# Performance work log

Measured on AMD Instinct MI355X. Metric: run time of the kernel, lower is better.

Reference implementation:

```python
import jax, jax.numpy as jnp
import numpy as np

B, S, E, H, D = 64, 512, 512, 8, 64  # batch, n_steps, embedding_size, head_count, QKV_dim

def setup_inputs() -> dict:
    key = jax.random.key(0)
    ks = jax.random.split(key, 7)
    x = jax.random.normal(ks[0], (B, S, E), dtype=jnp.float32)
    mask = jax.random.randint(ks[1], (B, S), 0, 2).astype(jnp.float32)  # 1 = masked out
    WQ = jax.random.normal(ks[2], (H, E, D), dtype=jnp.float32) * 0.1
    WK = jax.random.normal(ks[3], (H, E, D), dtype=jnp.float32) * 0.1
    WV = jax.random.normal(ks[4], (H, E, D), dtype=jnp.float32) * 0.1
    BE = jax.random.normal(ks[5], (S, E), dtype=jnp.float32) * 0.1
    WO = jax.random.normal(ks[6], (H * D, E), dtype=jnp.float32) * 0.1
    return {"x": x, "mask": mask, "WQ": WQ, "WK": WK, "WV": WV, "BE": BE, "WO": WO}

def reference(x, mask, WQ, WK, WV, BE, WO):
    # add learned positional bias
    h = x + BE  # [B,S,E]
    # per-head projections, vectorized over heads
    Q = jnp.einsum('bse,hed->bhsd', h, WQ)
    K = jnp.einsum('bse,hed->bhsd', h, WK)
    V = jnp.einsum('bse,hed->bhsd', h, WV)
    # NOTE: original scales by sqrt(embedding_size), not sqrt(QKV_dim)
    scores = jnp.einsum('bhsd,bhtd->bhst', Q, K) / np.sqrt(E).astype(np.float32)
    # additive mask trick: mask tiled over query dim, key positions masked where mask==1
    scores = scores - mask[:, None, None, :] * 1e10
    alpha = jax.nn.softmax(scores, axis=-1)  # [B,H,S,S]
    attn = jnp.einsum('bhst,bhtd->bhsd', alpha, V)  # [B,H,S,D]
    # concat heads along feature dim -> [B,S,H*D], then output projection
    attn = jnp.transpose(attn, (0, 2, 1, 3)).reshape(x.shape[0], x.shape[1], -1)
    return attn @ WO  # [B,S,E]
```

## Files before the change

### kernel.cpp

```cpp
#include <hip/hip_runtime.h>
#include <hip/hip_bf16.h>


#define Bn 64
#define Sn 512
#define En 512
#define Hn 8
#define Dn 64

typedef __attribute__((ext_vector_type(8))) short s8v;
typedef __attribute__((ext_vector_type(4))) float f4v;

__device__ __forceinline__ unsigned short f2bf(float f) {
    union { float f; unsigned int u; } v; v.f = f;
    unsigned int u = v.u;
    u += 0x7fffu + ((u >> 16) & 1u);
    return (unsigned short)(u >> 16);
}

__device__ __forceinline__ void async16(const unsigned short* g, unsigned short* l) {
    __builtin_amdgcn_global_load_lds((const __attribute__((address_space(1))) void*)g,
                                     (__attribute__((address_space(3))) void*)l, 16, 0, 0);
}
__device__ __forceinline__ void async4(const float* g, float* l) {
    __builtin_amdgcn_global_load_lds((const __attribute__((address_space(1))) void*)g,
                                     (__attribute__((address_space(3))) void*)l, 4, 0, 0);
}

__global__ __launch_bounds__(256) void prep_h(const float* __restrict__ x,
                                              const float* __restrict__ BE,
                                              unsigned short* __restrict__ hbf) {
    int i = (blockIdx.x * 256 + threadIdx.x) * 4;
    int se = i % (Sn * En);
    float4 a = *(const float4*)(x + i);
    float4 b = *(const float4*)(BE + se);
    ushort4 o;
    o.x = f2bf(a.x + b.x); o.y = f2bf(a.y + b.y);
    o.z = f2bf(a.z + b.z); o.w = f2bf(a.w + b.w);
    *(ushort4*)(hbf + i) = o;
}

__global__ __launch_bounds__(256) void prep_w(const float* __restrict__ WQ,
                                              const float* __restrict__ WK,
                                              const float* __restrict__ WV,
                                              const float* __restrict__ WO,
                                              unsigned short* __restrict__ Wqkvt,
                                              unsigned short* __restrict__ WOt) {
    int idx = blockIdx.x * 256 + threadIdx.x;
    const int NW = 3 * Hn * Dn * En;
    if (idx < NW) {
        int e = idx & 511;
        int d = (idx >> 9) & 63;
        int h = (idx >> 15) & 7;
        int m = idx >> 18;
        const float* W = (m == 0) ? WQ : (m == 1) ? WK : WV;
        Wqkvt[idx] = f2bf(W[(h * En + e) * Dn + d]);
    } else {
        int j = idx - NW;
        int n = j & 511;
        int e = j >> 9;
        WOt[j] = f2bf(WO[n * En + e]);
    }
}

__global__ __launch_bounds__(256) void qkv_gemm(const unsigned short* __restrict__ hbf,
                                                const unsigned short* __restrict__ Wqkvt,
                                                unsigned short* __restrict__ Qo,
                                                unsigned short* __restrict__ Ko,
                                                unsigned short* __restrict__ Vt) {
    int nb = blockIdx.x, mb = blockIdx.y;
    __shared__ __align__(16) unsigned short At[128 * 64];
    __shared__ __align__(16) unsigned short Bt[128 * 64];
    int tid = threadIdx.x;
    int w = tid >> 6, lane = tid & 63, quad = lane >> 4, l16 = lane & 15;
    int wr = w >> 1, wc = w & 1;
    int lrow = lane >> 3;
    int lseg = ((lane & 7) ^ lrow) * 8;

    f4v acc[4][4];
#pragma unroll
    for (int i = 0; i < 4; i++)
#pragma unroll
        for (int n = 0; n < 4; n++) acc[i][n] = (f4v){0.f, 0.f, 0.f, 0.f};

    const unsigned short* Ag = hbf + (size_t)mb * 128 * 512;
    const unsigned short* Bg = Wqkvt + (size_t)nb * 128 * 512;

    for (int kc = 0; kc < 8; kc++) {
        __syncthreads();
#pragma unroll
        for (int i = 0; i < 4; i++) {
            int r0 = w * 32 + i * 8;
            async16(Ag + (r0 + lrow) * 512 + kc * 64 + lseg, &At[r0 * 64]);
            async16(Bg + (r0 + lrow) * 512 + kc * 64 + lseg, &Bt[r0 * 64]);
        }
        __syncthreads();
#pragma unroll
        for (int ks = 0; ks < 2; ks++) {
            int sw = ((ks * 4 + quad) ^ (l16 & 7)) * 8;
            s8v a[4], b[4];
#pragma unroll
            for (int i = 0; i < 4; i++)
                a[i] = *(const s8v*)&At[(wr * 64 + i * 16 + l16) * 64 + sw];
#pragma unroll
            for (int n = 0; n < 4; n++)
                b[n] = *(const s8v*)&Bt[(wc * 64 + n * 16 + l16) * 64 + sw];
#pragma unroll
            for (int i = 0; i < 4; i++)
#pragma unroll
                for (int n = 0; n < 4; n++)
                    acc[i][n] = __builtin_amdgcn_mfma_f32_16x16x32_bf16(a[i], b[n], acc[i][n], 0, 0, 0);
        }
    }

    int mat = nb >> 2;
    int h = (nb & 3) * 2 + wc;
    int b = mb >> 2;
    int s0 = (mb & 3) * 128 + wr * 64;
    const float qscale = 0.06375873f;

    if (mat < 2) {
        unsigned short* op = (mat == 0) ? Qo : Ko;
        float sc = (mat == 0) ? qscale : 1.0f;
#pragma unroll
        for (int i = 0; i < 4; i++)
#pragma unroll
            for (int n = 0; n < 4; n++)
#pragma unroll
                for (int r = 0; r < 4; r++) {
                    int s = s0 + i * 16 + quad * 4 + r;
                    int d = n * 16 + l16;
                    op[(size_t)((b * Hn + h) * Sn + s) * Dn + d] = f2bf(acc[i][n][r] * sc);
                }
    } else {
#pragma unroll
        for (int i = 0; i < 4; i++)
#pragma unroll
            for (int n = 0; n < 4; n++) {
                int d = n * 16 + l16;
                int s = s0 + i * 16 + quad * 4;
                ushort4 pk;
                pk.x = f2bf(acc[i][n][0]); pk.y = f2bf(acc[i][n][1]);
                pk.z = f2bf(acc[i][n][2]); pk.w = f2bf(acc[i][n][3]);
                *(ushort4*)&Vt[(size_t)((b * Hn + h) * Dn + d) * Sn + s] = pk;
            }
    }
}

__global__ __launch_bounds__(512) void attn_kernel(const unsigned short* __restrict__ Q,
                                                   const unsigned short* __restrict__ K,
                                                   const unsigned short* __restrict__ Vt,
                                                   const float* __restrict__ mask,
                                                   unsigned short* __restrict__ attn) {
    int bh = blockIdx.x;
    int h = bh & 7, b = bh >> 3;
    __shared__ __align__(16) unsigned short Kc[64 * 64];
    __shared__ __align__(16) unsigned short Vc[64 * 64];
    __shared__ __align__(16) unsigned short Ps[8][16 * 64];
    __shared__ float maskv[64];
    int tid = threadIdx.x;
    int w = tid >> 6, lane = tid & 63, quad = lane >> 4, l16 = lane & 15;
    int l7 = l16 & 7, lh = l16 >> 3;
    int q4 = (quad & 1) * 4;

    const unsigned short* Qg = Q + (size_t)(bh * Sn) * Dn;
    const unsigned short* Kg = K + (size_t)(bh * Sn) * Dn;
    const unsigned short* Vg = Vt + (size_t)(bh * Dn) * Sn;

    s8v aq[4][2];
#pragma unroll
    for (int i = 0; i < 4; i++)
#pragma unroll
        for (int ks = 0; ks < 2; ks++)
            aq[i][ks] = *(const s8v*)&Qg[((w * 4 + i) * 16 + l16) * 64 + ks * 32 + quad * 8];

    f4v acc[4][4];
    float psum[4][4];
#pragma unroll
    for (int i = 0; i < 4; i++)
#pragma unroll
        for (int n = 0; n < 4; n++) {
            acc[i][n] = (f4v){0.f, 0.f, 0.f, 0.f};
            psum[i][n] = 0.f;
        }

    int srow = w * 8 + (lane >> 3);
    int sseg = ((lane & 7) ^ (srow & 7)) * 8;
    unsigned short* kdst = &Kc[w * 512];
    unsigned short* vdst = &Vc[w * 512];

    for (int kc = 0; kc < 8; kc++) {
        __syncthreads();
        async16(Kg + (kc * 64 + srow) * 64 + sseg, kdst);
        async16(Vg + srow * 512 + kc * 64 + sseg, vdst);
        if (w == 0) async4(mask + b * Sn + kc * 64 + lane, maskv);
        __syncthreads();

        unsigned short* Pw = Ps[w];
#pragma unroll
        for (int i = 0; i < 4; i++) {
            f4v sacc[4];
#pragma unroll
            for (int n = 0; n < 4; n++) sacc[n] = (f4v){0.f, 0.f, 0.f, 0.f};
#pragma unroll
            for (int ks = 0; ks < 2; ks++) {
                int sw = ((ks * 4 + quad) ^ l7) * 8;
#pragma unroll
                for (int n = 0; n < 4; n++) {
                    s8v bk = *(const s8v*)&Kc[(n * 16 + l16) * 64 + sw];
                    sacc[n] = __builtin_amdgcn_mfma_f32_16x16x32_bf16(aq[i][ks], bk, sacc[n], 0, 0, 0);
                }
            }
#pragma unroll
            for (int n = 0; n < 4; n++) {
                float msub = maskv[n * 16 + l16] * -1.4426950409e10f;
                int colpart = n * 2 + lh;
#pragma unroll
                for (int r = 0; r < 4; r++) {
                    float p = exp2f(sacc[n][r] + msub);
                    unsigned int u = __float_as_uint(p);
                    psum[i][r] += __uint_as_float(u & 0xffff0000u);
                    Pw[(quad * 4 + r) * 64 + ((colpart ^ (q4 + r)) * 8) + l7] =
                        (unsigned short)(u >> 16);
                }
            }
#pragma unroll
            for (int ks = 0; ks < 2; ks++) {
                int sw = ((ks * 4 + quad) ^ l7) * 8;
                s8v ap = *(const s8v*)&Pw[l16 * 64 + sw];
#pragma unroll
                for (int n = 0; n < 4; n++) {
                    s8v bv = *(const s8v*)&Vc[(n * 16 + l16) * 64 + sw];
                    acc[i][n] = __builtin_amdgcn_mfma_f32_16x16x32_bf16(ap, bv, acc[i][n], 0, 0, 0);
                }
            }
        }
    }

#pragma unroll
    for (int i = 0; i < 4; i++) {
        float inv[4];
#pragma unroll
        for (int r = 0; r < 4; r++) {
            float s = psum[i][r];
#pragma unroll
            for (int off = 1; off < 16; off <<= 1) s += __shfl_xor(s, off, 64);
            inv[r] = 1.0f / s;
        }
#pragma unroll
        for (int n = 0; n < 4; n++)
#pragma unroll
            for (int r = 0; r < 4; r++) {
                int query = (w * 4 + i) * 16 + quad * 4 + r;
                int col = h * 64 + n * 16 + l16;
                attn[(size_t)(b * Sn + query) * (Hn * Dn) + col] = f2bf(acc[i][n][r] * inv[r]);
            }
    }
}

__global__ __launch_bounds__(256) void outproj(const unsigned short* __restrict__ attn,
                                               const unsigned short* __restrict__ WOt,
                                               float* __restrict__ out) {
    int nb = blockIdx.x, mb = blockIdx.y;
    __shared__ __align__(16) unsigned short At[128 * 64];
    __shared__ __align__(16) unsigned short Bt[128 * 64];
    int tid = threadIdx.x;
    int w = tid >> 6, lane = tid & 63, quad = lane >> 4, l16 = lane & 15;
    int wr = w >> 1, wc = w & 1;
    int lrow = lane >> 3;
    int lseg = ((lane & 7) ^ lrow) * 8;

    f4v acc[4][4];
#pragma unroll
    for (int i = 0; i < 4; i++)
#pragma unroll
        for (int n = 0; n < 4; n++) acc[i][n] = (f4v){0.f, 0.f, 0.f, 0.f};

    const unsigned short* Ag = attn + (size_t)mb * 128 * 512;
    const unsigned short* Bg = WOt + (size_t)nb * 128 * 512;

    for (int kc = 0; kc < 8; kc++) {
        __syncthreads();
#pragma unroll
        for (int i = 0; i < 4; i++) {
            int r0 = w * 32 + i * 8;
            async16(Ag + (r0 + lrow) * 512 + kc * 64 + lseg, &At[r0 * 64]);
            async16(Bg + (r0 + lrow) * 512 + kc * 64 + lseg, &Bt[r0 * 64]);
        }
        __syncthreads();
#pragma unroll
        for (int ks = 0; ks < 2; ks++) {
            int sw = ((ks * 4 + quad) ^ (l16 & 7)) * 8;
            s8v a[4], b[4];
#pragma unroll
            for (int i = 0; i < 4; i++)
                a[i] = *(const s8v*)&At[(wr * 64 + i * 16 + l16) * 64 + sw];
#pragma unroll
            for (int n = 0; n < 4; n++)
                b[n] = *(const s8v*)&Bt[(wc * 64 + n * 16 + l16) * 64 + sw];
#pragma unroll
            for (int i = 0; i < 4; i++)
#pragma unroll
                for (int n = 0; n < 4; n++)
                    acc[i][n] = __builtin_amdgcn_mfma_f32_16x16x32_bf16(a[i], b[n], acc[i][n], 0, 0, 0);
        }
    }
#pragma unroll
    for (int i = 0; i < 4; i++)
#pragma unroll
        for (int n = 0; n < 4; n++)
#pragma unroll
            for (int r = 0; r < 4; r++) {
                int row = mb * 128 + wr * 64 + i * 16 + quad * 4 + r;
                int col = nb * 128 + wc * 64 + n * 16 + l16;
                out[(size_t)row * 512 + col] = acc[i][n][r];
            }
}

extern "C" void kernel_launch(void* const* d_in, const int* in_sizes, int n_in,
                              void* d_out, int out_size, void* d_ws, size_t ws_size,
                              hipStream_t stream) {
    const float* x    = (const float*)d_in[0];
    const float* mask = (const float*)d_in[1];
    const float* WQ   = (const float*)d_in[2];
    const float* WK   = (const float*)d_in[3];
    const float* WV   = (const float*)d_in[4];
    const float* BE   = (const float*)d_in[5];
    const float* WO   = (const float*)d_in[6];
    float* out = (float*)d_out;

    char* ws = (char*)d_ws;
    unsigned short* hbf   = (unsigned short*)(ws);
    unsigned short* Wqkvt = (unsigned short*)(ws + 33554432);
    unsigned short* WOt   = (unsigned short*)(ws + 35127296);
    unsigned short* Qp    = (unsigned short*)(ws + 35651584);
    unsigned short* Kp    = (unsigned short*)(ws + 69206016);
    unsigned short* Vtp   = (unsigned short*)(ws + 102760448);
    unsigned short* attnp = (unsigned short*)(ws + 136314880);

    prep_h<<<16384, 256, 0, stream>>>(x, BE, hbf);
    prep_w<<<4096, 256, 0, stream>>>(WQ, WK, WV, WO, Wqkvt, WOt);
    qkv_gemm<<<dim3(12, 256), 256, 0, stream>>>(hbf, Wqkvt, Qp, Kp, Vtp);
    attn_kernel<<<Bn * Hn, 512, 0, stream>>>(Qp, Kp, Vtp, mask, attnp);
    outproj<<<dim3(4, 256), 256, 0, stream>>>(attnp, WOt, out);
}
```

Baseline: 327.7 us.

## Split attention queries across two blocks and compute transposed scores for vectorized P stores

Runs the attention kernel as two 256-thread blocks per batch-head, each covering half of the queries, so there are more, smaller blocks. QK^T is computed with K as the A operand, which gives each lane four consecutive key columns. That lets P be written with packed 8-byte stores and the mask be read as a float4. K fragments are loaded once per chunk and reused across four query tiles, V fragments are reused across the four query tiles in the PV step, and the row-sum reduction needs fewer shuffles. In exchange, K and V are loaded twice per batch-head, once by each block, and register and LDS pressure rise from holding four P tiles per wave.

```diff
diff --git a/kernel.cpp b/kernel.cpp
--- a/kernel.cpp
+++ b/kernel.cpp
@@ -147,23 +147,22 @@
     }
 }
 
-__global__ __launch_bounds__(512) void attn_kernel(const unsigned short* __restrict__ Q,
+__global__ __launch_bounds__(256) void attn_kernel(const unsigned short* __restrict__ Q,
                                                    const unsigned short* __restrict__ K,
                                                    const unsigned short* __restrict__ Vt,
                                                    const float* __restrict__ mask,
                                                    unsigned short* __restrict__ attn) {
-    int bh = blockIdx.x;
+    int qhalf = blockIdx.x, bh = blockIdx.y;
     int h = bh & 7, b = bh >> 3;
     __shared__ __align__(16) unsigned short Kc[64 * 64];
     __shared__ __align__(16) unsigned short Vc[64 * 64];
-    __shared__ __align__(16) unsigned short Ps[8][16 * 64];
+    __shared__ __align__(16) unsigned short Ps[4][4 * 16 * 64];
     __shared__ float maskv[64];
     int tid = threadIdx.x;
     int w = tid >> 6, lane = tid & 63, quad = lane >> 4, l16 = lane & 15;
-    int l7 = l16 & 7, lh = l16 >> 3;
-    int q4 = (quad & 1) * 4;
-
-    const unsigned short* Qg = Q + (size_t)(bh * Sn) * Dn;
+    int l7 = l16 & 7;
+
+    const unsigned short* Qg = Q + (size_t)(bh * Sn + qhalf * 256) * Dn;
     const unsigned short* Kg = K + (size_t)(bh * Sn) * Dn;
     const unsigned short* Vg = Vt + (size_t)(bh * Dn) * Sn;
 
@@ -175,83 +174,95 @@
             aq[i][ks] = *(const s8v*)&Qg[((w * 4 + i) * 16 + l16) * 64 + ks * 32 + quad * 8];
 
     f4v acc[4][4];
-    float psum[4][4];
-#pragma unroll
-    for (int i = 0; i < 4; i++)
+    float psum[4] = {0.f, 0.f, 0.f, 0.f};
+#pragma unroll
+    for (int i = 0; i < 4; i++)
+#pragma unroll
+        for (int n = 0; n < 4; n++) acc[i][n] = (f4v){0.f, 0.f, 0.f, 0.f};
+
+    int srow0 = w * 16 + (lane >> 3);
+    int srow1 = srow0 + 8;
+    int gseg0 = ((lane & 7) ^ (srow0 & 7)) * 8;
+    int gseg1 = ((lane & 7) ^ (srow1 & 7)) * 8;
+    unsigned short* kdst0 = &Kc[(w * 16) * 64];
+    unsigned short* kdst1 = &Kc[(w * 16 + 8) * 64];
+    unsigned short* vdst0 = &Vc[(w * 16) * 64];
+    unsigned short* vdst1 = &Vc[(w * 16 + 8) * 64];
+
+    unsigned short* Pw = Ps[w];
+    int wbase = l16 * 64 + (quad & 1) * 4;
+    const float cM = -1.4426950409e10f;
+
+    for (int kc = 0; kc < 8; kc++) {
+        __syncthreads();
+        async16(Kg + (kc * 64 + srow0) * 64 + gseg0, kdst0);
+        async16(Kg + (kc * 64 + srow1) * 64 + gseg1, kdst1);
+        async16(Vg + srow0 * 512 + kc * 64 + gseg0, vdst0);
+        async16(Vg + srow1 * 512 + kc * 64 + gseg1, vdst1);
+        if (w == 0) async4(mask + b * Sn + kc * 64 + lane, maskv);
+        __syncthreads();
+
 #pragma unroll
         for (int n = 0; n < 4; n++) {
-            acc[i][n] = (f4v){0.f, 0.f, 0.f, 0.f};
-            psum[i][n] = 0.f;
-        }
-
-    int srow = w * 8 + (lane >> 3);
-    int sseg = ((lane & 7) ^ (srow & 7)) * 8;
-    unsigned short* kdst = &Kc[w * 512];
-    unsigned short* vdst = &Vc[w * 512];
-
-    for (int kc = 0; kc < 8; kc++) {
-        __syncthreads();
-        async16(Kg + (kc * 64 + srow) * 64 + sseg, kdst);
-        async16(Vg + srow * 512 + kc * 64 + sseg, vdst);
-        if (w == 0) async4(mask + b * Sn + kc * 64 + lane, maskv);
-        __syncthreads();
-
-        unsigned short* Pw = Ps[w];
-#pragma unroll
-        for (int i = 0; i < 4; i++) {
+            s8v bk0 = *(const s8v*)&Kc[(n * 16 + l16) * 64 + (quad ^ l7) * 8];
+            s8v bk1 = *(const s8v*)&Kc[(n * 16 + l16) * 64 + ((4 + quad) ^ l7) * 8];
+            float4 mv = *(const float4*)&maskv[n * 16 + quad * 4];
+            float m0 = mv.x * cM, m1 = mv.y * cM, m2 = mv.z * cM, m3 = mv.w * cM;
+            int wseg = ((n * 2 + (quad >> 1)) ^ l7) * 8;
             f4v sacc[4];
 #pragma unroll
-            for (int n = 0; n < 4; n++) sacc[n] = (f4v){0.f, 0.f, 0.f, 0.f};
-#pragma unroll
-            for (int ks = 0; ks < 2; ks++) {
-                int sw = ((ks * 4 + quad) ^ l7) * 8;
-#pragma unroll
-                for (int n = 0; n < 4; n++) {
-                    s8v bk = *(const s8v*)&Kc[(n * 16 + l16) * 64 + sw];
-                    sacc[n] = __builtin_amdgcn_mfma_f32_16x16x32_bf16(aq[i][ks], bk, sacc[n], 0, 0, 0);
-                }
-            }
+            for (int i = 0; i < 4; i++) {
+                sacc[i] = __builtin_amdgcn_mfma_f32_16x16x32_bf16(
+                              bk0, aq[i][0], (f4v){0.f, 0.f, 0.f, 0.f}, 0, 0, 0);
+                sacc[i] = __builtin_amdgcn_mfma_f32_16x16x32_bf16(
+                              bk1, aq[i][1], sacc[i], 0, 0, 0);
+            }
+#pragma unroll
+            for (int i = 0; i < 4; i++) {
+                unsigned int u0 = __float_as_uint(__builtin_amdgcn_exp2f(sacc[i][0] + m0));
+                unsigned int u1 = __float_as_uint(__builtin_amdgcn_exp2f(sacc[i][1] + m1));
+                unsigned int u2 = __float_as_uint(__builtin_amdgcn_exp2f(sacc[i][2] + m2));
+                unsigned int u3 = __float_as_uint(__builtin_amdgcn_exp2f(sacc[i][3] + m3));
+                psum[i] += __uint_as_float(u0 & 0xffff0000u) + __uint_as_float(u1 & 0xffff0000u)
+                         + __uint_as_float(u2 & 0xffff0000u) + __uint_as_float(u3 & 0xffff0000u);
+                uint2 pk;
+                pk.x = (u0 >> 16) | (u1 & 0xffff0000u);
+                pk.y = (u2 >> 16) | (u3 & 0xffff0000u);
+                *(uint2*)&Pw[(i << 10) + wbase + wseg] = pk;
+            }
+        }
+
+#pragma unroll
+        for (int ks = 0; ks < 2; ks++) {
+            int sw = ((ks * 4 + quad) ^ l7) * 8;
+            s8v ap[4];
+#pragma unroll
+            for (int i = 0; i < 4; i++)
+                ap[i] = *(const s8v*)&Pw[(i << 10) + l16 * 64 + sw];
 #pragma unroll
             for (int n = 0; n < 4; n++) {
-                float msub = maskv[n * 16 + l16] * -1.4426950409e10f;
-                int colpart = n * 2 + lh;
-#pragma unroll
-                for (int r = 0; r < 4; r++) {
-                    float p = exp2f(sacc[n][r] + msub);
-                    unsigned int u = __float_as_uint(p);
-                    psum[i][r] += __uint_as_float(u & 0xffff0000u);
-                    Pw[(quad * 4 + r) * 64 + ((colpart ^ (q4 + r)) * 8) + l7] =
-                        (unsigned short)(u >> 16);
-                }
-            }
-#pragma unroll
-            for (int ks = 0; ks < 2; ks++) {
-                int sw = ((ks * 4 + quad) ^ l7) * 8;
-                s8v ap = *(const s8v*)&Pw[l16 * 64 + sw];
-#pragma unroll
-                for (int n = 0; n < 4; n++) {
-                    s8v bv = *(const s8v*)&Vc[(n * 16 + l16) * 64 + sw];
-                    acc[i][n] = __builtin_amdgcn_mfma_f32_16x16x32_bf16(ap, bv, acc[i][n], 0, 0, 0);
-                }
+                s8v bv = *(const s8v*)&Vc[(n * 16 + l16) * 64 + sw];
+#pragma unroll
+                for (int i = 0; i < 4; i++)
+                    acc[i][n] = __builtin_amdgcn_mfma_f32_16x16x32_bf16(ap[i], bv, acc[i][n], 0, 0, 0);
             }
         }
     }
 
 #pragma unroll
     for (int i = 0; i < 4; i++) {
+        float s = psum[i];
+        s += __shfl_xor(s, 16, 64);
+        s += __shfl_xor(s, 32, 64);
         float inv[4];
 #pragma unroll
-        for (int r = 0; r < 4; r++) {
-            float s = psum[i][r];
-#pragma unroll
-            for (int off = 1; off < 16; off <<= 1) s += __shfl_xor(s, off, 64);
-            inv[r] = 1.0f / s;
-        }
+        for (int r = 0; r < 4; r++)
+            inv[r] = 1.0f / __shfl(s, quad * 4 + r, 64);
 #pragma unroll
         for (int n = 0; n < 4; n++)
 #pragma unroll
             for (int r = 0; r < 4; r++) {
-                int query = (w * 4 + i) * 16 + quad * 4 + r;
+                int query = qhalf * 256 + (w * 4 + i) * 16 + quad * 4 + r;
                 int col = h * 64 + n * 16 + l16;
                 attn[(size_t)(b * Sn + query) * (Hn * Dn) + col] = f2bf(acc[i][n][r] * inv[r]);
             }
@@ -341,6 +352,6 @@
     prep_h<<<16384, 256, 0, stream>>>(x, BE, hbf);
     prep_w<<<4096, 256, 0, stream>>>(WQ, WK, WV, WO, Wqkvt, WOt);
     qkv_gemm<<<dim3(12, 256), 256, 0, stream>>>(hbf, Wqkvt, Qp, Kp, Vtp);
-    attn_kernel<<<Bn * Hn, 512, 0, stream>>>(Qp, Kp, Vtp, mask, attnp);
+    attn_kernel<<<dim3(2, 512), 256, 0, stream>>>(Qp, Kp, Vtp, mask, attnp);
     outproj<<<dim3(4, 256), 256, 0, stream>>>(attnp, WOt, out);
 }
```

Result: faster. 296.3 us (-9.6%).
